# Kernel optimization log

Measured on AMD Instinct MI355X. Metric: run time of the kernel, lower is better.

## Reference

```python
import jax, jax.numpy as jnp
import numpy as np

D_IN = 256
DIMS = 256


def setup_inputs() -> dict:
    key = jax.random.key(0)
    k1, k2, k3, k4, k5 = jax.random.split(key, 5)
    B, Tq, Tk = 4, 512, 512
    query = jax.random.normal(k1, (B, Tq, D_IN), dtype=jnp.float32)
    value = jax.random.normal(k2, (B, Tk, D_IN), dtype=jnp.float32)
    # Dense(dims, use_bias=False) kernels (glorot-like scale) and AdditiveAttention scale vector
    Wq = jax.random.normal(k3, (D_IN, DIMS), dtype=jnp.float32) / np.sqrt(D_IN)
    Wv = jax.random.normal(k4, (D_IN, DIMS), dtype=jnp.float32) / np.sqrt(D_IN)
    scale = jax.random.normal(k5, (DIMS,), dtype=jnp.float32)
    return {"query": query, "value": value, "Wq": Wq, "Wv": Wv, "scale": scale}


def reference(query, value, Wq, Wv, scale):
    # q_proj: [B,Tq,d], k_proj: [B,Tk,d]; attention value = RAW value tensor (as in source)
    q = jnp.einsum("bqi,id->bqd", query, Wq)
    k = jnp.einsum("bki,id->bkd", value, Wv)
    # Additive (Bahdanau) scores: [B,Tq,Tk] via broadcast tanh then reduce with scale
    scores = jnp.einsum("bqkd,d->bqk", jnp.tanh(q[:, :, None, :] + k[:, None, :, :]), scale)
    attn = jax.nn.softmax(scores, axis=-1)  # masks are all-ones -> no-op
    out = jnp.einsum("bqk,bki->bqi", attn, value)
    return out, attn
```

## Files before the change

kernel.cpp:

```cpp
#include <hip/hip_runtime.h>

#define LOG2E 1.4426950408889634f
#define TWO_LOG2E 2.885390081777927f

__device__ __forceinline__ float fast_exp2(float x) { return __builtin_amdgcn_exp2f(x); }
__device__ __forceinline__ float fast_rcp(float x)  { return __builtin_amdgcn_rcpf(x); }

__device__ __forceinline__ void term2(float s0, float s1, float qx, float qy,
                                      float kx, float ky, float& acc) {
    const float A = fmaf(qx, kx, 1.f);
    const float B = fmaf(qy, ky, 1.f);
    acc = fmaf(fmaf(s1, A, s0 * B), fast_rcp(A * B), acc);
}

__global__ __launch_bounds__(256) void proj_kernel(
    const float* __restrict__ query, const float* __restrict__ value,
    const float* __restrict__ Wq, const float* __restrict__ Wv,
    float* __restrict__ eq, float* __restrict__ ek)
{
    __shared__ float in_lds[8 * 256];
    const int t = threadIdx.x;
    const int row0 = blockIdx.x * 8;
    const float* src; const float* W; float* dst;
    if (row0 < 2048) { src = query + (size_t)row0 * 256; W = Wq; dst = eq + (size_t)row0 * 256; }
    else { const int r = row0 - 2048; src = value + (size_t)r * 256; W = Wv; dst = ek + (size_t)r * 256; }

    const float4* s4 = (const float4*)src;
    float4* l4 = (float4*)in_lds;
    l4[t] = s4[t];
    l4[t + 256] = s4[t + 256];
    __syncthreads();

    float acc[8];
#pragma unroll
    for (int r = 0; r < 8; ++r) acc[r] = 0.f;

    for (int d = 0; d < 256; d += 4) {
        const float w0 = W[(d + 0) * 256 + t];
        const float w1 = W[(d + 1) * 256 + t];
        const float w2 = W[(d + 2) * 256 + t];
        const float w3 = W[(d + 3) * 256 + t];
#pragma unroll
        for (int r = 0; r < 8; ++r) {
            const float4 v = *(const float4*)&in_lds[r * 256 + d];
            acc[r] = fmaf(v.x, w0, acc[r]);
            acc[r] = fmaf(v.y, w1, acc[r]);
            acc[r] = fmaf(v.z, w2, acc[r]);
            acc[r] = fmaf(v.w, w3, acc[r]);
        }
    }
#pragma unroll
    for (int r = 0; r < 8; ++r) dst[r * 256 + t] = fast_exp2(acc[r] * TWO_LOG2E);
}

#define EK_ST 260
#define EQ_ST 260
#define SS_ST 520
__global__ __launch_bounds__(512) void fused_kernel(
    const float* __restrict__ eq, const float* __restrict__ ek,
    const float* __restrict__ scale, const float* __restrict__ value,
    float* __restrict__ attn, float* __restrict__ out)
{
    __shared__ float ek_lds[64 * EK_ST];
    __shared__ float eq_lds[8 * EQ_ST];
    __shared__ float sc_lds[256];
    __shared__ float s_tile[8 * SS_ST];
    __shared__ float pslot[8 * SS_ST];
    __shared__ float inv_lds[8];

    const int t = threadIdx.x;
    const int w = t >> 6, lane = t & 63;
    const int qp = lane >> 4;
    const int kq = lane & 15;
    const int ds = 32 * w;
    const int qt = blockIdx.x, b = blockIdx.y;
    const int q0 = qt * 8;

    const float* ekb = ek + (size_t)(b * 512) * 256;

    {
        const int row = t >> 6, c = t & 63;
        const float4 v = ((const float4*)(eq + (size_t)(b * 512 + q0) * 256))[row * 64 + c];
        *(float4*)&eq_lds[row * EQ_ST + 4 * c] = v;
    }
    if (t < 256) sc_lds[t] = -2.f * scale[t];
    {
        const float4* src = (const float4*)ekb;
#pragma unroll
        for (int l = 0; l < 8; ++l) {
            const int row = 8 * l + w;
            const int cc = 4 * ((lane + (row >> 2)) & 63);
            *(float4*)&ek_lds[row * EK_ST + cc] = src[row * 64 + lane];
        }
    }
    __syncthreads();

#pragma unroll
    for (int tt = 0; tt < 8; ++tt) {
        float a00 = 0.f, a01 = 0.f, a02 = 0.f, a03 = 0.f;
        float a10 = 0.f, a11 = 0.f, a12 = 0.f, a13 = 0.f;

#pragma unroll
        for (int it = 0; it < 8; ++it) {
            const int d = ds + 4 * it;
            const float4 sv = *(const float4*)&sc_lds[d];
            const float4 q0v = *(const float4*)&eq_lds[(2 * qp + 0) * EQ_ST + d];
            const float4 q1v = *(const float4*)&eq_lds[(2 * qp + 1) * EQ_ST + d];
            const int cc = 4 * (((d >> 2) + kq) & 63);
            const float4 k0 = *(const float4*)&ek_lds[(4 * kq + 0) * EK_ST + cc];
            const float4 k1 = *(const float4*)&ek_lds[(4 * kq + 1) * EK_ST + cc];
            const float4 k2 = *(const float4*)&ek_lds[(4 * kq + 2) * EK_ST + cc];
            const float4 k3 = *(const float4*)&ek_lds[(4 * kq + 3) * EK_ST + cc];

            term2(sv.x, sv.y, q0v.x, q0v.y, k0.x, k0.y, a00);
            term2(sv.x, sv.y, q0v.x, q0v.y, k1.x, k1.y, a01);
            term2(sv.x, sv.y, q0v.x, q0v.y, k2.x, k2.y, a02);
            term2(sv.x, sv.y, q0v.x, q0v.y, k3.x, k3.y, a03);
            term2(sv.x, sv.y, q1v.x, q1v.y, k0.x, k0.y, a10);
            term2(sv.x, sv.y, q1v.x, q1v.y, k1.x, k1.y, a11);
            term2(sv.x, sv.y, q1v.x, q1v.y, k2.x, k2.y, a12);
            term2(sv.x, sv.y, q1v.x, q1v.y, k3.x, k3.y, a13);

            term2(sv.z, sv.w, q0v.z, q0v.w, k0.z, k0.w, a00);
            term2(sv.z, sv.w, q0v.z, q0v.w, k1.z, k1.w, a01);
            term2(sv.z, sv.w, q0v.z, q0v.w, k2.z, k2.w, a02);
            term2(sv.z, sv.w, q0v.z, q0v.w, k3.z, k3.w, a03);
            term2(sv.z, sv.w, q1v.z, q1v.w, k0.z, k0.w, a10);
            term2(sv.z, sv.w, q1v.z, q1v.w, k1.z, k1.w, a11);
            term2(sv.z, sv.w, q1v.z, q1v.w, k2.z, k2.w, a12);
            term2(sv.z, sv.w, q1v.z, q1v.w, k3.z, k3.w, a13);
        }

        {
            float* ps = &pslot[w * SS_ST];
            const int s0i = (2 * qp + 0) * 64 + 4 * kq;
            const int s1i = (2 * qp + 1) * 64 + 4 * kq;
            ps[s0i + 0] = a00; ps[s0i + 1] = a01; ps[s0i + 2] = a02; ps[s0i + 3] = a03;
            ps[s1i + 0] = a10; ps[s1i + 1] = a11; ps[s1i + 2] = a12; ps[s1i + 3] = a13;
        }
        __syncthreads();

        if (tt < 7) {
            const float4* src = (const float4*)(ekb + (size_t)(64 * (tt + 1)) * 256);
#pragma unroll
            for (int l = 0; l < 8; ++l) {
                const int row = 8 * l + w;
                const int cc = 4 * ((lane + (row >> 2)) & 63);
                *(float4*)&ek_lds[row * EK_ST + cc] = src[row * 64 + lane];
            }
        }
        {
            float s = pslot[t];
#pragma unroll
            for (int o = 1; o < 8; ++o) s += pslot[o * SS_ST + t];
            s_tile[(t >> 6) * SS_ST + 64 * tt + (t & 63)] = s;
        }
        __syncthreads();
    }

    float x[8];
    float m = -1e30f;
#pragma unroll
    for (int j = 0; j < 8; ++j) {
        x[j] = s_tile[w * SS_ST + 64 * j + lane];
        m = fmaxf(m, x[j]);
    }
#pragma unroll
    for (int off = 32; off; off >>= 1) m = fmaxf(m, __shfl_xor(m, off));

    float sum = 0.f;
#pragma unroll
    for (int j = 0; j < 8; ++j) { x[j] = fast_exp2((x[j] - m) * LOG2E); sum += x[j]; }
#pragma unroll
    for (int off = 32; off; off >>= 1) sum += __shfl_xor(sum, off);
    const float inv = fast_rcp(sum);

    float* arow = attn + (size_t)(b * 512 + q0 + w) * 512;
#pragma unroll
    for (int j = 0; j < 8; ++j) {
        s_tile[w * SS_ST + 64 * j + lane] = x[j];
        arow[64 * j + lane] = x[j] * inv;
    }
    if (lane == 0) inv_lds[w] = inv;
    __syncthreads();

    float4 acc[8];
#pragma unroll
    for (int r = 0; r < 8; ++r) acc[r] = make_float4(0.f, 0.f, 0.f, 0.f);

    const float* vbase = value + (size_t)(b * 512 + 64 * w) * 256;
    for (int k4 = 0; k4 < 64; k4 += 4) {
        const float4 v0 = *(const float4*)&vbase[(k4 + 0) * 256 + lane * 4];
        const float4 v1 = *(const float4*)&vbase[(k4 + 1) * 256 + lane * 4];
        const float4 v2 = *(const float4*)&vbase[(k4 + 2) * 256 + lane * 4];
        const float4 v3 = *(const float4*)&vbase[(k4 + 3) * 256 + lane * 4];
#pragma unroll
        for (int r = 0; r < 8; ++r) {
            const float4 s4 = *(const float4*)&s_tile[r * SS_ST + 64 * w + k4];
            acc[r].x = fmaf(s4.x, v0.x, acc[r].x); acc[r].y = fmaf(s4.x, v0.y, acc[r].y);
            acc[r].z = fmaf(s4.x, v0.z, acc[r].z); acc[r].w = fmaf(s4.x, v0.w, acc[r].w);
            acc[r].x = fmaf(s4.y, v1.x, acc[r].x); acc[r].y = fmaf(s4.y, v1.y, acc[r].y);
            acc[r].z = fmaf(s4.y, v1.z, acc[r].z); acc[r].w = fmaf(s4.y, v1.w, acc[r].w);
            acc[r].x = fmaf(s4.z, v2.x, acc[r].x); acc[r].y = fmaf(s4.z, v2.y, acc[r].y);
            acc[r].z = fmaf(s4.z, v2.z, acc[r].z); acc[r].w = fmaf(s4.z, v2.w, acc[r].w);
            acc[r].x = fmaf(s4.w, v3.x, acc[r].x); acc[r].y = fmaf(s4.w, v3.y, acc[r].y);
            acc[r].z = fmaf(s4.w, v3.z, acc[r].z); acc[r].w = fmaf(s4.w, v3.w, acc[r].w);
        }
    }

    float* red = ek_lds;
    if (w >= 4) {
#pragma unroll
        for (int r = 0; r < 8; ++r)
            *(float4*)&red[((w - 4) * 8 + r) * 256 + lane * 4] = acc[r];
    }
    __syncthreads();
    if (w < 4) {
#pragma unroll
        for (int r = 0; r < 8; ++r) {
            const float4 o = *(const float4*)&red[(w * 8 + r) * 256 + lane * 4];
            acc[r].x += o.x; acc[r].y += o.y; acc[r].z += o.z; acc[r].w += o.w;
        }
    }
    __syncthreads();
    if (w >= 2 && w < 4) {
#pragma unroll
        for (int r = 0; r < 8; ++r)
            *(float4*)&red[((w - 2) * 8 + r) * 256 + lane * 4] = acc[r];
    }
    __syncthreads();
    if (w < 2) {
#pragma unroll
        for (int r = 0; r < 8; ++r) {
            const float4 o = *(const float4*)&red[(w * 8 + r) * 256 + lane * 4];
            acc[r].x += o.x; acc[r].y += o.y; acc[r].z += o.z; acc[r].w += o.w;
        }
    }
    __syncthreads();
    if (w == 1) {
#pragma unroll
        for (int r = 0; r < 8; ++r)
            *(float4*)&red[r * 256 + lane * 4] = acc[r];
    }
    __syncthreads();
    if (w == 0) {
#pragma unroll
        for (int r = 0; r < 8; ++r) {
            const float4 o = *(const float4*)&red[r * 256 + lane * 4];
            const float iv = inv_lds[r];
            float4 res;
            res.x = (acc[r].x + o.x) * iv;
            res.y = (acc[r].y + o.y) * iv;
            res.z = (acc[r].z + o.z) * iv;
            res.w = (acc[r].w + o.w) * iv;
            *(float4*)&out[(size_t)(b * 512 + q0 + r) * 256 + lane * 4] = res;
        }
    }
}

extern "C" void kernel_launch(void* const* d_in, const int* in_sizes, int n_in,
                              void* d_out, int out_size, void* d_ws, size_t ws_size,
                              hipStream_t stream) {
    const float* query = (const float*)d_in[0];
    const float* value = (const float*)d_in[1];
    const float* Wq    = (const float*)d_in[2];
    const float* Wv    = (const float*)d_in[3];
    const float* scale = (const float*)d_in[4];

    float* out0 = (float*)d_out;
    float* attn = out0 + 4 * 512 * 256;

    float* eq = (float*)d_ws;
    float* ek = eq + 2048 * 256;

    proj_kernel<<<512, 256, 0, stream>>>(query, value, Wq, Wv, eq, ek);
    fused_kernel<<<dim3(64, 4), 512, 0, stream>>>(eq, ek, scale, value, attn, out0);
}
```

Before: 67.17 us.

## Split key tile staging into two d-halves to halve LDS footprint

The fused kernel now stages each 64-key tile of exp-projected keys in two 128-wide halves of the feature dimension instead of one full 256-wide tile. This roughly halves the key buffer in LDS so more blocks could fit per CU. The cost is extra __syncthreads per tile, and the key loads are no longer issued during the partial-sum reduction, so load latency is exposed inside the compute loop. With only 256 blocks in the grid, higher per-CU occupancy may not help.

```diff
diff --git a/kernel.cpp b/kernel.cpp
--- a/kernel.cpp
+++ b/kernel.cpp
@@ -53,7 +53,7 @@
     for (int r = 0; r < 8; ++r) dst[r * 256 + t] = fast_exp2(acc[r] * TWO_LOG2E);
 }
 
-#define EK_ST 260
+#define EKH_ST 132
 #define EQ_ST 260
 #define SS_ST 520
 __global__ __launch_bounds__(512) void fused_kernel(
@@ -61,7 +61,7 @@
     const float* __restrict__ scale, const float* __restrict__ value,
     float* __restrict__ attn, float* __restrict__ out)
 {
-    __shared__ float ek_lds[64 * EK_ST];
+    __shared__ float ek_lds[64 * EKH_ST];
     __shared__ float eq_lds[8 * EQ_ST];
     __shared__ float sc_lds[256];
     __shared__ float s_tile[8 * SS_ST];
@@ -72,11 +72,10 @@
     const int w = t >> 6, lane = t & 63;
     const int qp = lane >> 4;
     const int kq = lane & 15;
-    const int ds = 32 * w;
     const int qt = blockIdx.x, b = blockIdx.y;
     const int q0 = qt * 8;
 
-    const float* ekb = ek + (size_t)(b * 512) * 256;
+    const float4* ekb4 = (const float4*)(ek + (size_t)(b * 512) * 256);
 
     {
         const int row = t >> 6, c = t & 63;
@@ -84,51 +83,55 @@
         *(float4*)&eq_lds[row * EQ_ST + 4 * c] = v;
     }
     if (t < 256) sc_lds[t] = -2.f * scale[t];
-    {
-        const float4* src = (const float4*)ekb;
-#pragma unroll
-        for (int l = 0; l < 8; ++l) {
-            const int row = 8 * l + w;
-            const int cc = 4 * ((lane + (row >> 2)) & 63);
-            *(float4*)&ek_lds[row * EK_ST + cc] = src[row * 64 + lane];
-        }
-    }
-    __syncthreads();
-
-#pragma unroll
+
     for (int tt = 0; tt < 8; ++tt) {
         float a00 = 0.f, a01 = 0.f, a02 = 0.f, a03 = 0.f;
         float a10 = 0.f, a11 = 0.f, a12 = 0.f, a13 = 0.f;
 
 #pragma unroll
-        for (int it = 0; it < 8; ++it) {
-            const int d = ds + 4 * it;
-            const float4 sv = *(const float4*)&sc_lds[d];
-            const float4 q0v = *(const float4*)&eq_lds[(2 * qp + 0) * EQ_ST + d];
-            const float4 q1v = *(const float4*)&eq_lds[(2 * qp + 1) * EQ_ST + d];
-            const int cc = 4 * (((d >> 2) + kq) & 63);
-            const float4 k0 = *(const float4*)&ek_lds[(4 * kq + 0) * EK_ST + cc];
-            const float4 k1 = *(const float4*)&ek_lds[(4 * kq + 1) * EK_ST + cc];
-            const float4 k2 = *(const float4*)&ek_lds[(4 * kq + 2) * EK_ST + cc];
-            const float4 k3 = *(const float4*)&ek_lds[(4 * kq + 3) * EK_ST + cc];
-
-            term2(sv.x, sv.y, q0v.x, q0v.y, k0.x, k0.y, a00);
-            term2(sv.x, sv.y, q0v.x, q0v.y, k1.x, k1.y, a01);
-            term2(sv.x, sv.y, q0v.x, q0v.y, k2.x, k2.y, a02);
-            term2(sv.x, sv.y, q0v.x, q0v.y, k3.x, k3.y, a03);
-            term2(sv.x, sv.y, q1v.x, q1v.y, k0.x, k0.y, a10);
-            term2(sv.x, sv.y, q1v.x, q1v.y, k1.x, k1.y, a11);
-            term2(sv.x, sv.y, q1v.x, q1v.y, k2.x, k2.y, a12);
-            term2(sv.x, sv.y, q1v.x, q1v.y, k3.x, k3.y, a13);
-
-            term2(sv.z, sv.w, q0v.z, q0v.w, k0.z, k0.w, a00);
-            term2(sv.z, sv.w, q0v.z, q0v.w, k1.z, k1.w, a01);
-            term2(sv.z, sv.w, q0v.z, q0v.w, k2.z, k2.w, a02);
-            term2(sv.z, sv.w, q0v.z, q0v.w, k3.z, k3.w, a03);
-            term2(sv.z, sv.w, q1v.z, q1v.w, k0.z, k0.w, a10);
-            term2(sv.z, sv.w, q1v.z, q1v.w, k1.z, k1.w, a11);
-            term2(sv.z, sv.w, q1v.z, q1v.w, k2.z, k2.w, a12);
-            term2(sv.z, sv.w, q1v.z, q1v.w, k3.z, k3.w, a13);
+        for (int h = 0; h < 2; ++h) {
+            __syncthreads();
+#pragma unroll
+            for (int l = 0; l < 4; ++l) {
+                const int idx = t + 512 * l;
+                const int row = idx >> 5, c = idx & 31;
+                const int cc = (c + (row >> 2)) & 31;
+                *(float4*)&ek_lds[row * EKH_ST + 4 * cc] =
+                    ekb4[(size_t)(64 * tt + row) * 64 + 32 * h + c];
+            }
+            __syncthreads();
+
+#pragma unroll
+            for (int it = 0; it < 4; ++it) {
+                const int dl = 16 * w + 4 * it;
+                const int dg = 128 * h + dl;
+                const float4 sv  = *(const float4*)&sc_lds[dg];
+                const float4 q0v = *(const float4*)&eq_lds[(2 * qp + 0) * EQ_ST + dg];
+                const float4 q1v = *(const float4*)&eq_lds[(2 * qp + 1) * EQ_ST + dg];
+                const int cc = 4 * (((dl >> 2) + kq) & 31);
+                const float4 k0 = *(const float4*)&ek_lds[(4 * kq + 0) * EKH_ST + cc];
+                const float4 k1 = *(const float4*)&ek_lds[(4 * kq + 1) * EKH_ST + cc];
+                const float4 k2 = *(const float4*)&ek_lds[(4 * kq + 2) * EKH_ST + cc];
+                const float4 k3 = *(const float4*)&ek_lds[(4 * kq + 3) * EKH_ST + cc];
+
+                term2(sv.x, sv.y, q0v.x, q0v.y, k0.x, k0.y, a00);
+                term2(sv.x, sv.y, q0v.x, q0v.y, k1.x, k1.y, a01);
+                term2(sv.x, sv.y, q0v.x, q0v.y, k2.x, k2.y, a02);
+                term2(sv.x, sv.y, q0v.x, q0v.y, k3.x, k3.y, a03);
+                term2(sv.x, sv.y, q1v.x, q1v.y, k0.x, k0.y, a10);
+                term2(sv.x, sv.y, q1v.x, q1v.y, k1.x, k1.y, a11);
+                term2(sv.x, sv.y, q1v.x, q1v.y, k2.x, k2.y, a12);
+                term2(sv.x, sv.y, q1v.x, q1v.y, k3.x, k3.y, a13);
+
+                term2(sv.z, sv.w, q0v.z, q0v.w, k0.z, k0.w, a00);
+                term2(sv.z, sv.w, q0v.z, q0v.w, k1.z, k1.w, a01);
+                term2(sv.z, sv.w, q0v.z, q0v.w, k2.z, k2.w, a02);
+                term2(sv.z, sv.w, q0v.z, q0v.w, k3.z, k3.w, a03);
+                term2(sv.z, sv.w, q1v.z, q1v.w, k0.z, k0.w, a10);
+                term2(sv.z, sv.w, q1v.z, q1v.w, k1.z, k1.w, a11);
+                term2(sv.z, sv.w, q1v.z, q1v.w, k2.z, k2.w, a12);
+                term2(sv.z, sv.w, q1v.z, q1v.w, k3.z, k3.w, a13);
+            }
         }
 
         {
@@ -139,24 +142,14 @@
             ps[s1i + 0] = a10; ps[s1i + 1] = a11; ps[s1i + 2] = a12; ps[s1i + 3] = a13;
         }
         __syncthreads();
-
-        if (tt < 7) {
-            const float4* src = (const float4*)(ekb + (size_t)(64 * (tt + 1)) * 256);
-#pragma unroll
-            for (int l = 0; l < 8; ++l) {
-                const int row = 8 * l + w;
-                const int cc = 4 * ((lane + (row >> 2)) & 63);
-                *(float4*)&ek_lds[row * EK_ST + cc] = src[row * 64 + lane];
-            }
-        }
         {
             float s = pslot[t];
 #pragma unroll
             for (int o = 1; o < 8; ++o) s += pslot[o * SS_ST + t];
             s_tile[(t >> 6) * SS_ST + 64 * tt + (t & 63)] = s;
         }
-        __syncthreads();
-    }
+    }
+    __syncthreads();
 
     float x[8];
     float m = -1e30f;
```

Result: slower. 69.12 us (+2.9%).

## Double fused kernel block to 1024 threads, splitting d-range and keys per wave

Applied to the files above, without the earlier changes.

Launches the fused attention kernel with 1024 threads instead of 512. In the score phase each wave pair covers one 32-wide slice of d, with the two half-waves splitting it further and combining through a lane shuffle. In the PV phase each wave handles 32 keys instead of 64, and an extra reduction stage is added. The goal is more waves per CU to hide latency, since the grid has only 256 blocks. The cost is extra shuffles and syncs, and a tighter per-thread register budget.

```diff
diff --git a/kernel.cpp b/kernel.cpp
--- a/kernel.cpp
+++ b/kernel.cpp
@@ -56,7 +56,8 @@
 #define EK_ST 260
 #define EQ_ST 260
 #define SS_ST 520
-__global__ __launch_bounds__(512) void fused_kernel(
+#define PS_ST 520
+__global__ __launch_bounds__(1024) void fused_kernel(
     const float* __restrict__ eq, const float* __restrict__ ek,
     const float* __restrict__ scale, const float* __restrict__ value,
     float* __restrict__ attn, float* __restrict__ out)
@@ -65,47 +66,49 @@
     __shared__ float eq_lds[8 * EQ_ST];
     __shared__ float sc_lds[256];
     __shared__ float s_tile[8 * SS_ST];
-    __shared__ float pslot[8 * SS_ST];
+    __shared__ float pslot[8 * PS_ST];
     __shared__ float inv_lds[8];
 
     const int t = threadIdx.x;
     const int w = t >> 6, lane = t & 63;
-    const int qp = lane >> 4;
-    const int kq = lane & 15;
-    const int ds = 32 * w;
+    const int oct = w >> 1, qh = w & 1;
+    const int dd = lane >> 5, qp = (lane >> 4) & 1, kq = lane & 15;
     const int qt = blockIdx.x, b = blockIdx.y;
     const int q0 = qt * 8;
 
-    const float* ekb = ek + (size_t)(b * 512) * 256;
-
-    {
+    const float4* ekb4 = (const float4*)(ek + (size_t)(b * 512) * 256);
+
+    if (t < 512) {
         const int row = t >> 6, c = t & 63;
         const float4 v = ((const float4*)(eq + (size_t)(b * 512 + q0) * 256))[row * 64 + c];
         *(float4*)&eq_lds[row * EQ_ST + 4 * c] = v;
-    }
-    if (t < 256) sc_lds[t] = -2.f * scale[t];
+    } else if (t < 768) {
+        sc_lds[t - 512] = -2.f * scale[t - 512];
+    }
     {
-        const float4* src = (const float4*)ekb;
-#pragma unroll
-        for (int l = 0; l < 8; ++l) {
-            const int row = 8 * l + w;
-            const int cc = 4 * ((lane + (row >> 2)) & 63);
-            *(float4*)&ek_lds[row * EK_ST + cc] = src[row * 64 + lane];
-        }
-    }
-    __syncthreads();
-
-#pragma unroll
+#pragma unroll
+        for (int l = 0; l < 4; ++l) {
+            const int row = w + 16 * l;
+            const int cc = (lane + (row >> 2)) & 63;
+            *(float4*)&ek_lds[row * EK_ST + 4 * cc] = ekb4[(size_t)row * 64 + lane];
+        }
+    }
+    __syncthreads();
+
+    const int qr0 = 4 * qh + 2 * qp;
+    const float* eqr0 = &eq_lds[(qr0 + 0) * EQ_ST];
+    const float* eqr1 = &eq_lds[(qr0 + 1) * EQ_ST];
+
     for (int tt = 0; tt < 8; ++tt) {
         float a00 = 0.f, a01 = 0.f, a02 = 0.f, a03 = 0.f;
         float a10 = 0.f, a11 = 0.f, a12 = 0.f, a13 = 0.f;
 
 #pragma unroll
-        for (int it = 0; it < 8; ++it) {
-            const int d = ds + 4 * it;
-            const float4 sv = *(const float4*)&sc_lds[d];
-            const float4 q0v = *(const float4*)&eq_lds[(2 * qp + 0) * EQ_ST + d];
-            const float4 q1v = *(const float4*)&eq_lds[(2 * qp + 1) * EQ_ST + d];
+        for (int it = 0; it < 4; ++it) {
+            const int d = 32 * oct + 16 * dd + 4 * it;
+            const float4 sv  = *(const float4*)&sc_lds[d];
+            const float4 q0v = *(const float4*)&eqr0[d];
+            const float4 q1v = *(const float4*)&eqr1[d];
             const int cc = 4 * (((d >> 2) + kq) & 63);
             const float4 k0 = *(const float4*)&ek_lds[(4 * kq + 0) * EK_ST + cc];
             const float4 k1 = *(const float4*)&ek_lds[(4 * kq + 1) * EK_ST + cc];
@@ -131,72 +134,79 @@
             term2(sv.z, sv.w, q1v.z, q1v.w, k3.z, k3.w, a13);
         }
 
-        {
-            float* ps = &pslot[w * SS_ST];
-            const int s0i = (2 * qp + 0) * 64 + 4 * kq;
-            const int s1i = (2 * qp + 1) * 64 + 4 * kq;
+        a00 += __shfl_xor(a00, 32); a01 += __shfl_xor(a01, 32);
+        a02 += __shfl_xor(a02, 32); a03 += __shfl_xor(a03, 32);
+        a10 += __shfl_xor(a10, 32); a11 += __shfl_xor(a11, 32);
+        a12 += __shfl_xor(a12, 32); a13 += __shfl_xor(a13, 32);
+
+        if (dd == 0) {
+            float* ps = &pslot[oct * PS_ST];
+            const int s0i = (qr0 + 0) * 64 + 4 * kq;
+            const int s1i = (qr0 + 1) * 64 + 4 * kq;
             ps[s0i + 0] = a00; ps[s0i + 1] = a01; ps[s0i + 2] = a02; ps[s0i + 3] = a03;
             ps[s1i + 0] = a10; ps[s1i + 1] = a11; ps[s1i + 2] = a12; ps[s1i + 3] = a13;
         }
         __syncthreads();
 
         if (tt < 7) {
-            const float4* src = (const float4*)(ekb + (size_t)(64 * (tt + 1)) * 256);
-#pragma unroll
-            for (int l = 0; l < 8; ++l) {
-                const int row = 8 * l + w;
-                const int cc = 4 * ((lane + (row >> 2)) & 63);
-                *(float4*)&ek_lds[row * EK_ST + cc] = src[row * 64 + lane];
+            const float4* src = ekb4 + (size_t)(64 * (tt + 1)) * 64;
+#pragma unroll
+            for (int l = 0; l < 4; ++l) {
+                const int row = w + 16 * l;
+                const int cc = (lane + (row >> 2)) & 63;
+                *(float4*)&ek_lds[row * EK_ST + 4 * cc] = src[(size_t)row * 64 + lane];
             }
         }
-        {
+        if (t < 512) {
             float s = pslot[t];
 #pragma unroll
-            for (int o = 1; o < 8; ++o) s += pslot[o * SS_ST + t];
+            for (int o = 1; o < 8; ++o) s += pslot[o * PS_ST + t];
             s_tile[(t >> 6) * SS_ST + 64 * tt + (t & 63)] = s;
         }
         __syncthreads();
     }
 
-    float x[8];
-    float m = -1e30f;
-#pragma unroll
-    for (int j = 0; j < 8; ++j) {
-        x[j] = s_tile[w * SS_ST + 64 * j + lane];
-        m = fmaxf(m, x[j]);
-    }
-#pragma unroll
-    for (int off = 32; off; off >>= 1) m = fmaxf(m, __shfl_xor(m, off));
-
-    float sum = 0.f;
-#pragma unroll
-    for (int j = 0; j < 8; ++j) { x[j] = fast_exp2((x[j] - m) * LOG2E); sum += x[j]; }
-#pragma unroll
-    for (int off = 32; off; off >>= 1) sum += __shfl_xor(sum, off);
-    const float inv = fast_rcp(sum);
-
-    float* arow = attn + (size_t)(b * 512 + q0 + w) * 512;
-#pragma unroll
-    for (int j = 0; j < 8; ++j) {
-        s_tile[w * SS_ST + 64 * j + lane] = x[j];
-        arow[64 * j + lane] = x[j] * inv;
-    }
-    if (lane == 0) inv_lds[w] = inv;
+    if (w < 8) {
+        float x[8];
+        float m = -1e30f;
+#pragma unroll
+        for (int j = 0; j < 8; ++j) {
+            x[j] = s_tile[w * SS_ST + 64 * j + lane];
+            m = fmaxf(m, x[j]);
+        }
+#pragma unroll
+        for (int off = 32; off; off >>= 1) m = fmaxf(m, __shfl_xor(m, off));
+
+        float sum = 0.f;
+#pragma unroll
+        for (int j = 0; j < 8; ++j) { x[j] = fast_exp2((x[j] - m) * LOG2E); sum += x[j]; }
+#pragma unroll
+        for (int off = 32; off; off >>= 1) sum += __shfl_xor(sum, off);
+        const float inv = fast_rcp(sum);
+
+        float* arow = attn + (size_t)(b * 512 + q0 + w) * 512;
+#pragma unroll
+        for (int j = 0; j < 8; ++j) {
+            s_tile[w * SS_ST + 64 * j + lane] = x[j];
+            arow[64 * j + lane] = x[j] * inv;
+        }
+        if (lane == 0) inv_lds[w] = inv;
+    }
     __syncthreads();
 
     float4 acc[8];
 #pragma unroll
     for (int r = 0; r < 8; ++r) acc[r] = make_float4(0.f, 0.f, 0.f, 0.f);
 
-    const float* vbase = value + (size_t)(b * 512 + 64 * w) * 256;
-    for (int k4 = 0; k4 < 64; k4 += 4) {
+    const float* vbase = value + (size_t)(b * 512 + 32 * w) * 256;
+    for (int k4 = 0; k4 < 32; k4 += 4) {
         const float4 v0 = *(const float4*)&vbase[(k4 + 0) * 256 + lane * 4];
         const float4 v1 = *(const float4*)&vbase[(k4 + 1) * 256 + lane * 4];
         const float4 v2 = *(const float4*)&vbase[(k4 + 2) * 256 + lane * 4];
         const float4 v3 = *(const float4*)&vbase[(k4 + 3) * 256 + lane * 4];
 #pragma unroll
         for (int r = 0; r < 8; ++r) {
-            const float4 s4 = *(const float4*)&s_tile[r * SS_ST + 64 * w + k4];
+            const float4 s4 = *(const float4*)&s_tile[r * SS_ST + 32 * w + k4];
             acc[r].x = fmaf(s4.x, v0.x, acc[r].x); acc[r].y = fmaf(s4.x, v0.y, acc[r].y);
             acc[r].z = fmaf(s4.x, v0.z, acc[r].z); acc[r].w = fmaf(s4.x, v0.w, acc[r].w);
             acc[r].x = fmaf(s4.y, v1.x, acc[r].x); acc[r].y = fmaf(s4.y, v1.y, acc[r].y);
@@ -209,7 +219,21 @@
     }
 
     float* red = ek_lds;
-    if (w >= 4) {
+    if (w >= 8) {
+#pragma unroll
+        for (int r = 0; r < 8; ++r)
+            *(float4*)&red[((w - 8) * 8 + r) * 256 + lane * 4] = acc[r];
+    }
+    __syncthreads();
+    if (w < 8) {
+#pragma unroll
+        for (int r = 0; r < 8; ++r) {
+            const float4 o = *(const float4*)&red[(w * 8 + r) * 256 + lane * 4];
+            acc[r].x += o.x; acc[r].y += o.y; acc[r].z += o.z; acc[r].w += o.w;
+        }
+    }
+    __syncthreads();
+    if (w >= 4 && w < 8) {
 #pragma unroll
         for (int r = 0; r < 8; ++r)
             *(float4*)&red[((w - 4) * 8 + r) * 256 + lane * 4] = acc[r];
@@ -274,5 +298,5 @@
     float* ek = eq + 2048 * 256;
 
     proj_kernel<<<512, 256, 0, stream>>>(query, value, Wq, Wv, eq, ek);
-    fused_kernel<<<dim3(64, 4), 512, 0, stream>>>(eq, ek, scale, value, attn, out0);
+    fused_kernel<<<dim3(64, 4), 1024, 0, stream>>>(eq, ek, scale, value, attn, out0);
 }
```

Measured after the change: 67.59 us. No clear change (+0.6%).
